# Optimization experiments

Hardware: AMD Instinct MI355X
Metric: run time of the kernel (lower is better)

## Reference

```python
import jax, jax.numpy as jnp
import numpy as np

N, E, H, NH, CUTOFF = 20000, 320000, 128, 8, 5.0
HD = H // NH
EPS = 1e-8
act = jax.nn.silu


def setup_inputs() -> dict:
    key = jax.random.key(0)
    ks = jax.random.split(key, 20)
    g = 1.0 / np.sqrt(H)
    return {
        'node_scalar': jax.random.normal(ks[0], (N, H), jnp.float32),
        'node_vector': jax.random.normal(ks[1], (N, 3, H), jnp.float32),
        'edge_index': jax.random.randint(ks[2], (2, E), 0, N),
        'dist': jax.random.uniform(ks[3], (E,), jnp.float32) * CUTOFF,
        'edge_feats': jax.random.normal(ks[4], (E, H), jnp.float32),
        'edge_vector': jax.random.normal(ks[5], (E, 3), jnp.float32),
        'ln_gamma': jnp.ones((H,), jnp.float32),
        'ln_beta': jnp.zeros((H,), jnp.float32),
        'alpha': jax.random.normal(ks[6], (1, NH, HD), jnp.float32) * g,
        'W_cross': jax.random.normal(ks[7], (H, H), jnp.float32) * g,
        'W_node': jax.random.normal(ks[8], (H, H), jnp.float32) * g,
        'b_node': jnp.zeros((H,), jnp.float32),
        'W_edge': jax.random.normal(ks[9], (H, H), jnp.float32) * g,
        'b_edge': jnp.zeros((H,), jnp.float32),
        'W_p1': jax.random.normal(ks[10], (H, 2 * H), jnp.float32) * g,
        'b_p1': jnp.zeros((2 * H,), jnp.float32),
        'W_p2': jax.random.normal(ks[11], (H, 3 * H), jnp.float32) * g,
        'b_p2': jnp.zeros((3 * H,), jnp.float32),
        'W_vec': jax.random.normal(ks[12], (H, 2 * H), jnp.float32) * g,
        'W_f': jax.random.normal(ks[13], (H, H), jnp.float32) * g,
        'b_f': jnp.zeros((H,), jnp.float32),
    }


def _layernorm(x, gamma, beta):
    mu = jnp.mean(x, axis=-1, keepdims=True)
    var = jnp.var(x, axis=-1, keepdims=True)
    return (x - mu) * jax.lax.rsqrt(var + 1e-5) * gamma + beta


def _cutoff(d):
    return 0.5 * (jnp.cos(jnp.pi * d / CUTOFF) + 1.0) * (d < CUTOFF).astype(d.dtype)


def reference(node_scalar, node_vector, edge_index, dist, edge_feats, edge_vector,
              ln_gamma, ln_beta, alpha, W_cross, W_node, b_node, W_edge, b_edge,
              W_p1, b_p1, W_p2, b_p2, W_vec, W_f, b_f):
    i, j = edge_index[0], edge_index[1]

    scalar_out = _layernorm(node_scalar, ln_gamma, ln_beta)

    # ---- message ----
    ef = act(edge_feats @ W_edge + b_edge).reshape(E, NH, HD)
    ns = (scalar_out @ W_node + b_node).reshape(N, NH, HD)
    attn = act(ns[i] + ns[j] + ef) * alpha            # [E,NH,HD]
    attn = attn.sum(-1) * _cutoff(dist)[:, None]      # [E,NH]
    msg = (ns[j] * ef * attn[:, :, None]).reshape(E, H)
    s1, s2 = jnp.split(act(msg @ W_p1 + b_p1), 2, axis=1)
    vmsg = node_vector[j] * s1[:, None, :] + s2[:, None, :] * edge_vector[:, :, None]
    scalar_agg = jax.ops.segment_sum(msg, i, num_segments=N)
    vector_agg = jax.ops.segment_sum(vmsg, i, num_segments=N)

    # ---- edge update ----
    nv = node_vector @ W_cross                        # [N,3,H]
    ci = jnp.cross(nv[i], edge_vector[:, :, None], axis=1)
    cj = jnp.cross(nv[j], edge_vector[:, :, None], axis=1)
    sum_phi = (ci * cj).sum(1)                        # [E,H]
    edge_feats_out = edge_feats + act(edge_feats @ W_f + b_f) * sum_phi

    node_scalar = node_scalar + scalar_agg
    node_vector = node_vector + vector_agg

    # ---- node update ----
    v1, v2 = jnp.split(node_vector @ W_vec, 2, axis=-1)  # [N,3,H] each
    vec_tri = (v1 * v2).sum(1)                           # [N,H]
    norm_vec = jnp.sqrt((v2 ** 2).sum(-2) + EPS)
    vec_qua = norm_vec ** 3
    p1, p2, p3 = jnp.split(node_scalar @ W_p2 + b_p2, 3, axis=1)
    delta_scalar = (vec_qua + vec_tri) * p1 + p2
    delta_vector = v1 * p3[:, None, :]

    node_scalar = node_scalar + delta_scalar
    node_vector = node_vector + delta_vector
    return node_scalar, node_vector, edge_feats_out
```

## Files before the change

### kernel.cpp

```cpp
#include <hip/hip_runtime.h>

#define N_NODES 20000
#define N_EDGES 320000
#define HDIM    128
#define PI_F    3.14159265358979323846f
#define CUTOFF_R 5.0f

__device__ __forceinline__ float silu_f(float x) {
    return x / (1.0f + __expf(-x));
}

__global__ __launch_bounds__(256) void ln_kernel(
    const float* __restrict__ x, const float* __restrict__ gamma,
    const float* __restrict__ beta, float* __restrict__ out)
{
    int row  = blockIdx.x * 4 + (threadIdx.x >> 6);
    int lane = threadIdx.x & 63;
    if (row >= N_NODES) return;
    const float* xr = x + row * HDIM;
    float x0 = xr[lane], x1 = xr[lane + 64];
    float s  = x0 + x1;
    float s2 = x0 * x0 + x1 * x1;
#pragma unroll
    for (int m = 32; m >= 1; m >>= 1) {
        s  += __shfl_xor(s,  m, 64);
        s2 += __shfl_xor(s2, m, 64);
    }
    float mean = s * (1.0f / 128.0f);
    float var  = s2 * (1.0f / 128.0f) - mean * mean;
    float rstd = rsqrtf(var + 1e-5f);
    out[row * HDIM + lane]      = (x0 - mean) * rstd * gamma[lane]      + beta[lane];
    out[row * HDIM + lane + 64] = (x1 - mean) * rstd * gamma[lane + 64] + beta[lane + 64];
}

template <bool SILU, bool BIAS>
__global__ __launch_bounds__(256) void gemm_k128(
    const float* __restrict__ A, const float* __restrict__ W,
    const float* __restrict__ bias, float* __restrict__ out,
    int M, int C)
{
    __shared__ float As[64][33];
    __shared__ float Ws[32][128];

    int tid = threadIdx.x;
    int tx = tid & 15, ty = tid >> 4;
    int m0 = blockIdx.x * 64;
    int n0 = blockIdx.y * 128;

    float acc[4][8];
#pragma unroll
    for (int r = 0; r < 4; ++r)
#pragma unroll
        for (int c = 0; c < 8; ++c) acc[r][c] = 0.0f;

    for (int k0 = 0; k0 < 128; k0 += 32) {
        __syncthreads();
#pragma unroll
        for (int p = 0; p < 2; ++p) {
            int f  = tid + p * 256;
            int ar = f >> 3, k4 = (f & 7) * 4;
            int gr = m0 + ar;
            float4 v = (gr < M) ? *(const float4*)&A[gr * 128 + k0 + k4]
                                : make_float4(0.f, 0.f, 0.f, 0.f);
            As[ar][k4 + 0] = v.x; As[ar][k4 + 1] = v.y;
            As[ar][k4 + 2] = v.z; As[ar][k4 + 3] = v.w;
        }
#pragma unroll
        for (int p = 0; p < 4; ++p) {
            int f  = tid + p * 256;
            int kr = f >> 5, c4 = (f & 31) * 4;
            *(float4*)&Ws[kr][c4] = *(const float4*)&W[(k0 + kr) * C + n0 + c4];
        }
        __syncthreads();
#pragma unroll 8
        for (int k = 0; k < 32; ++k) {
            float av[4];
#pragma unroll
            for (int r = 0; r < 4; ++r) av[r] = As[ty * 4 + r][k];
            float4 w0 = *(float4*)&Ws[k][tx * 8];
            float4 w1 = *(float4*)&Ws[k][tx * 8 + 4];
            float wv[8] = {w0.x, w0.y, w0.z, w0.w, w1.x, w1.y, w1.z, w1.w};
#pragma unroll
            for (int r = 0; r < 4; ++r)
#pragma unroll
                for (int c = 0; c < 8; ++c) acc[r][c] += av[r] * wv[c];
        }
    }
#pragma unroll
    for (int r = 0; r < 4; ++r) {
        int gr = m0 + ty * 4 + r;
        if (gr < M) {
            float res[8];
#pragma unroll
            for (int c = 0; c < 8; ++c) {
                float v = acc[r][c];
                if (BIAS) v += bias[n0 + tx * 8 + c];
                if (SILU) v = silu_f(v);
                res[c] = v;
            }
            *(float4*)&out[gr * C + n0 + tx * 8]     = make_float4(res[0], res[1], res[2], res[3]);
            *(float4*)&out[gr * C + n0 + tx * 8 + 4] = make_float4(res[4], res[5], res[6], res[7]);
        }
    }
}

__global__ __launch_bounds__(256) void edge_msg_kernel(
    float* __restrict__ efmsg, const float* __restrict__ ns,
    const int* __restrict__ eidx, const float* __restrict__ dist,
    const float* __restrict__ alpha, float* __restrict__ sagg)
{
    int e = blockIdx.x * 2 + (threadIdx.x >> 7);
    int h = threadIdx.x & 127;
    int i = eidx[e], j = eidx[N_EDGES + e];
    float ef  = efmsg[e * HDIM + h];
    float nsi = ns[i * HDIM + h];
    float nsj = ns[j * HDIM + h];
    float pre = silu_f(nsi + nsj + ef) * alpha[h];
#pragma unroll
    for (int m = 8; m >= 1; m >>= 1) pre += __shfl_xor(pre, m, 16);
    float d   = dist[e];
    float cut = (d < CUTOFF_R) ? 0.5f * (cosf(PI_F * d * (1.0f / CUTOFF_R)) + 1.0f) : 0.0f;
    float msg = nsj * ef * (pre * cut);
    efmsg[e * HDIM + h] = msg;
    atomicAdd(&sagg[i * HDIM + h], msg);
}

__global__ __launch_bounds__(256) void gemm_p1_vmsg(
    const float* __restrict__ Amsg, const float* __restrict__ Wp1,
    const float* __restrict__ bp1, const float* __restrict__ node_vector,
    const int* __restrict__ eidx, const float* __restrict__ edge_vector,
    float* __restrict__ vagg)
{
    __shared__ float As[32][33];
    __shared__ float Ws[32][256];
    __shared__ int   ei_s[32], ej_s[32];
    __shared__ float ev_s[32][3];

    int tid = threadIdx.x;
    int tx = tid & 31, ty = tid >> 5;
    int e0 = blockIdx.x * 32;

    if (tid < 32) { ei_s[tid] = eidx[e0 + tid]; ej_s[tid] = eidx[N_EDGES + e0 + tid]; }
    if (tid >= 64 && tid < 160) {
        int t = tid - 64;
        ev_s[t / 3][t % 3] = edge_vector[e0 * 3 + t];
    }

    float acc[4][8];
#pragma unroll
    for (int r = 0; r < 4; ++r)
#pragma unroll
        for (int c = 0; c < 8; ++c) acc[r][c] = 0.0f;

    for (int k0 = 0; k0 < 128; k0 += 32) {
        __syncthreads();
        {
            int ar = tid >> 3, k4 = (tid & 7) * 4;
            float4 v = *(const float4*)&Amsg[(e0 + ar) * 128 + k0 + k4];
            As[ar][k4 + 0] = v.x; As[ar][k4 + 1] = v.y;
            As[ar][k4 + 2] = v.z; As[ar][k4 + 3] = v.w;
        }
#pragma unroll
        for (int p = 0; p < 8; ++p) {
            int f  = tid + p * 256;
            int kr = f >> 6, c4 = (f & 63) * 4;
            *(float4*)&Ws[kr][c4] = *(const float4*)&Wp1[(k0 + kr) * 256 + c4];
        }
        __syncthreads();
#pragma unroll 8
        for (int k = 0; k < 32; ++k) {
            float av[4];
#pragma unroll
            for (int r = 0; r < 4; ++r) av[r] = As[ty * 4 + r][k];
            float4 w0 = *(float4*)&Ws[k][tx * 8];
            float4 w1 = *(float4*)&Ws[k][tx * 8 + 4];
            float wv[8] = {w0.x, w0.y, w0.z, w0.w, w1.x, w1.y, w1.z, w1.w};
#pragma unroll
            for (int r = 0; r < 4; ++r)
#pragma unroll
                for (int c = 0; c < 8; ++c) acc[r][c] += av[r] * wv[c];
        }
    }
    __syncthreads();
#pragma unroll
    for (int r = 0; r < 4; ++r)
#pragma unroll
        for (int c = 0; c < 8; ++c)
            Ws[ty * 4 + r][tx * 8 + c] = silu_f(acc[r][c] + bp1[tx * 8 + c]);
    __syncthreads();

#pragma unroll
    for (int p = 0; p < 16; ++p) {
        int idx = tid + p * 256;
        int r = idx >> 7, h = idx & 127;
        float s1 = Ws[r][h], s2 = Ws[r][h + 128];
        int i = ei_s[r], j = ej_s[r];
#pragma unroll
        for (int d = 0; d < 3; ++d) {
            float v = node_vector[(j * 3 + d) * 128 + h] * s1 + s2 * ev_s[r][d];
            atomicAdd(&vagg[(i * 3 + d) * 128 + h], v);
        }
    }
}

__global__ __launch_bounds__(256) void gemm_wf_edgeout(
    const float* __restrict__ edge_feats, const float* __restrict__ Wf,
    const float* __restrict__ bf, const float* __restrict__ nvg,
    const int* __restrict__ eidx, const float* __restrict__ edge_vector,
    float* __restrict__ edge_out)
{
    __shared__ float As[64][33];
    __shared__ float Ws[32][128];
    __shared__ int   ei_s[64], ej_s[64];
    __shared__ float ev_s[64][3];

    int tid = threadIdx.x;
    int tx = tid & 15, ty = tid >> 4;
    int e0 = blockIdx.x * 64;

    if (tid < 64) { ei_s[tid] = eidx[e0 + tid]; ej_s[tid] = eidx[N_EDGES + e0 + tid]; }
    if (tid >= 64 && tid < 256) {
        int t = tid - 64;
        if (t < 192) ev_s[t / 3][t % 3] = edge_vector[e0 * 3 + t];
    }

    float acc[4][8];
#pragma unroll
    for (int r = 0; r < 4; ++r)
#pragma unroll
        for (int c = 0; c < 8; ++c) acc[r][c] = 0.0f;

    for (int k0 = 0; k0 < 128; k0 += 32) {
        __syncthreads();
#pragma unroll
        for (int p = 0; p < 2; ++p) {
            int f  = tid + p * 256;
            int ar = f >> 3, k4 = (f & 7) * 4;
            float4 v = *(const float4*)&edge_feats[(e0 + ar) * 128 + k0 + k4];
            As[ar][k4 + 0] = v.x; As[ar][k4 + 1] = v.y;
            As[ar][k4 + 2] = v.z; As[ar][k4 + 3] = v.w;
        }
#pragma unroll
        for (int p = 0; p < 4; ++p) {
            int f  = tid + p * 256;
            int kr = f >> 5, c4 = (f & 31) * 4;
            *(float4*)&Ws[kr][c4] = *(const float4*)&Wf[(k0 + kr) * 128 + c4];
        }
        __syncthreads();
#pragma unroll 8
        for (int k = 0; k < 32; ++k) {
            float av[4];
#pragma unroll
            for (int r = 0; r < 4; ++r) av[r] = As[ty * 4 + r][k];
            float4 w0 = *(float4*)&Ws[k][tx * 8];
            float4 w1 = *(float4*)&Ws[k][tx * 8 + 4];
            float wv[8] = {w0.x, w0.y, w0.z, w0.w, w1.x, w1.y, w1.z, w1.w};
#pragma unroll
            for (int r = 0; r < 4; ++r)
#pragma unroll
                for (int c = 0; c < 8; ++c) acc[r][c] += av[r] * wv[c];
        }
    }

#pragma unroll
    for (int r = 0; r < 4; ++r) {
        int row = ty * 4 + r;
        int e   = e0 + row;
        int i = ei_s[row], j = ej_s[row];
        float ev0 = ev_s[row][0], ev1 = ev_s[row][1], ev2 = ev_s[row][2];
        float nvi[3][8], nvj[3][8];
#pragma unroll
        for (int d = 0; d < 3; ++d) {
            float4 a0 = *(const float4*)&nvg[(i * 3 + d) * 128 + tx * 8];
            float4 a1 = *(const float4*)&nvg[(i * 3 + d) * 128 + tx * 8 + 4];
            nvi[d][0] = a0.x; nvi[d][1] = a0.y; nvi[d][2] = a0.z; nvi[d][3] = a0.w;
            nvi[d][4] = a1.x; nvi[d][5] = a1.y; nvi[d][6] = a1.z; nvi[d][7] = a1.w;
            float4 b0 = *(const float4*)&nvg[(j * 3 + d) * 128 + tx * 8];
            float4 b1 = *(const float4*)&nvg[(j * 3 + d) * 128 + tx * 8 + 4];
            nvj[d][0] = b0.x; nvj[d][1] = b0.y; nvj[d][2] = b0.z; nvj[d][3] = b0.w;
            nvj[d][4] = b1.x; nvj[d][5] = b1.y; nvj[d][6] = b1.z; nvj[d][7] = b1.w;
        }
        float4 f0 = *(const float4*)&edge_feats[e * 128 + tx * 8];
        float4 f1 = *(const float4*)&edge_feats[e * 128 + tx * 8 + 4];
        float efres[8] = {f0.x, f0.y, f0.z, f0.w, f1.x, f1.y, f1.z, f1.w};
        float res[8];
#pragma unroll
        for (int c = 0; c < 8; ++c) {
            float ci0 = nvi[1][c] * ev2 - nvi[2][c] * ev1;
            float ci1 = nvi[2][c] * ev0 - nvi[0][c] * ev2;
            float ci2 = nvi[0][c] * ev1 - nvi[1][c] * ev0;
            float cj0 = nvj[1][c] * ev2 - nvj[2][c] * ev1;
            float cj1 = nvj[2][c] * ev0 - nvj[0][c] * ev2;
            float cj2 = nvj[0][c] * ev1 - nvj[1][c] * ev0;
            float sp  = ci0 * cj0 + ci1 * cj1 + ci2 * cj2;
            float t   = silu_f(acc[r][c] + bf[tx * 8 + c]);
            res[c] = efres[c] + t * sp;
        }
        *(float4*)&edge_out[e * 128 + tx * 8]     = make_float4(res[0], res[1], res[2], res[3]);
        *(float4*)&edge_out[e * 128 + tx * 8 + 4] = make_float4(res[4], res[5], res[6], res[7]);
    }
}

__global__ __launch_bounds__(256) void node_add_kernel(
    const float* __restrict__ ns0, const float* __restrict__ sagg,
    const float* __restrict__ nv0, const float* __restrict__ vagg,
    float* __restrict__ ns_new, float* __restrict__ nv_new)
{
    int idx = blockIdx.x * 256 + threadIdx.x;
    const int nsf4 = N_NODES * HDIM / 4;
    if (idx < nsf4) {
        float4 a = ((const float4*)ns0)[idx];
        float4 b = ((const float4*)sagg)[idx];
        ((float4*)ns_new)[idx] = make_float4(a.x + b.x, a.y + b.y, a.z + b.z, a.w + b.w);
    } else {
        int k = idx - nsf4;
        float4 a = ((const float4*)nv0)[k];
        float4 b = ((const float4*)vagg)[k];
        ((float4*)nv_new)[k] = make_float4(a.x + b.x, a.y + b.y, a.z + b.z, a.w + b.w);
    }
}

__global__ __launch_bounds__(256) void final_node_kernel(
    const float* __restrict__ v12, const float* __restrict__ p123,
    const float* __restrict__ ns_new, const float* __restrict__ nv_new,
    float* __restrict__ out_s, float* __restrict__ out_v)
{
    int idx = blockIdx.x * 256 + threadIdx.x;
    int n = idx >> 7, h = idx & 127;
    float tri = 0.f, q2 = 0.f;
    float v1d[3];
#pragma unroll
    for (int d = 0; d < 3; ++d) {
        float v1 = v12[(n * 3 + d) * 256 + h];
        float v2 = v12[(n * 3 + d) * 256 + 128 + h];
        v1d[d] = v1;
        tri += v1 * v2;
        q2  += v2 * v2;
    }
    float nrm = sqrtf(q2 + 1e-8f);
    float qua = nrm * nrm * nrm;
    float p1 = p123[n * 384 + h];
    float p2 = p123[n * 384 + 128 + h];
    float p3 = p123[n * 384 + 256 + h];
    out_s[idx] = ns_new[idx] + (qua + tri) * p1 + p2;
#pragma unroll
    for (int d = 0; d < 3; ++d)
        out_v[(n * 3 + d) * 128 + h] = nv_new[(n * 3 + d) * 128 + h] + v1d[d] * p3;
}

extern "C" void kernel_launch(void* const* d_in, const int* in_sizes, int n_in,
                              void* d_out, int out_size, void* d_ws, size_t ws_size,
                              hipStream_t stream)
{
    const float* node_scalar = (const float*)d_in[0];
    const float* node_vector = (const float*)d_in[1];
    const int*   edge_index  = (const int*)d_in[2];
    const float* dist        = (const float*)d_in[3];
    const float* edge_feats  = (const float*)d_in[4];
    const float* edge_vector = (const float*)d_in[5];
    const float* ln_gamma    = (const float*)d_in[6];
    const float* ln_beta     = (const float*)d_in[7];
    const float* alpha       = (const float*)d_in[8];
    const float* W_cross     = (const float*)d_in[9];
    const float* W_node      = (const float*)d_in[10];
    const float* b_node      = (const float*)d_in[11];
    const float* W_edge      = (const float*)d_in[12];
    const float* b_edge      = (const float*)d_in[13];
    const float* W_p1        = (const float*)d_in[14];
    const float* b_p1        = (const float*)d_in[15];
    const float* W_p2        = (const float*)d_in[16];
    const float* b_p2        = (const float*)d_in[17];
    const float* W_vec       = (const float*)d_in[18];
    const float* W_f         = (const float*)d_in[19];
    const float* b_f         = (const float*)d_in[20];

    float* out_scalar = (float*)d_out;
    float* out_vector = out_scalar + N_NODES * HDIM;
    float* out_edge   = out_vector + N_NODES * 3 * HDIM;

    float* ws         = (float*)d_ws;
    float* scalar_out = ws;
    float* ns         = scalar_out + 2560000;
    float* nv         = ns + 2560000;
    float* sagg       = nv + 7680000;
    float* vagg       = sagg + 2560000;
    float* efmsg      = vagg + 7680000;
    float* v12        = efmsg;
    float* p123       = efmsg + 15360000;

    hipMemsetAsync(sagg, 0, (size_t)(2560000 + 7680000) * sizeof(float), stream);

    hipLaunchKernelGGL(ln_kernel, dim3(5000), dim3(256), 0, stream,
                       node_scalar, ln_gamma, ln_beta, scalar_out);
    hipLaunchKernelGGL((gemm_k128<false, true>), dim3(313, 1), dim3(256), 0, stream,
                       scalar_out, W_node, b_node, ns, N_NODES, 128);
    hipLaunchKernelGGL((gemm_k128<false, false>), dim3(938, 1), dim3(256), 0, stream,
                       node_vector, W_cross, nullptr, nv, 3 * N_NODES, 128);

    hipLaunchKernelGGL((gemm_k128<true, true>), dim3(5000, 1), dim3(256), 0, stream,
                       edge_feats, W_edge, b_edge, efmsg, N_EDGES, 128);
    hipLaunchKernelGGL(edge_msg_kernel, dim3(160000), dim3(256), 0, stream,
                       efmsg, ns, edge_index, dist, alpha, sagg);
    hipLaunchKernelGGL(gemm_p1_vmsg, dim3(10000), dim3(256), 0, stream,
                       efmsg, W_p1, b_p1, node_vector, edge_index, edge_vector, vagg);
    hipLaunchKernelGGL(gemm_wf_edgeout, dim3(5000), dim3(256), 0, stream,
                       edge_feats, W_f, b_f, nv, edge_index, edge_vector, out_edge);

    hipLaunchKernelGGL(node_add_kernel, dim3(10000), dim3(256), 0, stream,
                       node_scalar, sagg, node_vector, vagg, scalar_out, nv);
    hipLaunchKernelGGL((gemm_k128<false, false>), dim3(938, 2), dim3(256), 0, stream,
                       nv, W_vec, nullptr, v12, 3 * N_NODES, 256);
    hipLaunchKernelGGL((gemm_k128<false, true>), dim3(313, 3), dim3(256), 0, stream,
                       scalar_out, W_p2, b_p2, p123, N_NODES, 384);
    hipLaunchKernelGGL(final_node_kernel, dim3(10000), dim3(256), 0, stream,
                       v12, p123, scalar_out, nv, out_scalar, out_vector);
}
```

Before: 1.560 ms.

## Sort edges by destination, fuse edge GEMM with message, pre-reduce atomics, enlarge GEMM tiles

```diff
diff --git a/kernel.cpp b/kernel.cpp
--- a/kernel.cpp
+++ b/kernel.cpp
@@ -6,8 +6,9 @@
 #define PI_F    3.14159265358979323846f
 #define CUTOFF_R 5.0f
 
-__device__ __forceinline__ float silu_f(float x) {
-    return x / (1.0f + __expf(-x));
+__device__ __forceinline__ float silu_f(float x) { return x / (1.0f + __expf(-x)); }
+__device__ __forceinline__ float cutoff_f(float d) {
+    return (d < CUTOFF_R) ? 0.5f * (__cosf(PI_F * d * (1.0f / CUTOFF_R)) + 1.0f) : 0.0f;
 }
 
 __global__ __launch_bounds__(256) void ln_kernel(
@@ -17,7 +18,7 @@
     int row  = blockIdx.x * 4 + (threadIdx.x >> 6);
     int lane = threadIdx.x & 63;
     if (row >= N_NODES) return;
-    const float* xr = x + row * HDIM;
+    const float* xr = x + (size_t)row * HDIM;
     float x0 = xr[lane], x1 = xr[lane + 64];
     float s  = x0 + x1;
     float s2 = x0 * x0 + x1 * x1;
@@ -33,256 +34,399 @@
     out[row * HDIM + lane + 64] = (x1 - mean) * rstd * gamma[lane + 64] + beta[lane + 64];
 }
 
-template <bool SILU, bool BIAS>
-__global__ __launch_bounds__(256) void gemm_k128(
+__global__ __launch_bounds__(256) void count_kernel(const int* __restrict__ ei, int* __restrict__ cnt) {
+    int e = blockIdx.x * 256 + threadIdx.x;
+    if (e < N_EDGES) atomicAdd(&cnt[ei[e]], 1);
+}
+
+__global__ __launch_bounds__(1024) void scan_kernel(const int* __restrict__ cnt, int* __restrict__ ofs) {
+    __shared__ int part[1024];
+    int tid = threadIdx.x;
+    const int PER = 20;
+    int base = tid * PER;
+    int s = 0;
+    for (int t = 0; t < PER; ++t) { int b = base + t; if (b < N_NODES) s += cnt[b]; }
+    part[tid] = s;
+    __syncthreads();
+    for (int off = 1; off < 1024; off <<= 1) {
+        int v = (tid >= off) ? part[tid - off] : 0;
+        __syncthreads();
+        part[tid] += v;
+        __syncthreads();
+    }
+    int run = (tid > 0) ? part[tid - 1] : 0;
+    for (int t = 0; t < PER; ++t) {
+        int b = base + t;
+        if (b < N_NODES) { ofs[b] = run; run += cnt[b]; }
+    }
+}
+
+__global__ __launch_bounds__(256) void scatter_kernel(const int* __restrict__ ei,
+                                                      int* __restrict__ ofs, int* __restrict__ perm) {
+    int e = blockIdx.x * 256 + threadIdx.x;
+    if (e < N_EDGES) { int p = atomicAdd(&ofs[ei[e]], 1); perm[p] = e; }
+}
+
+template <bool BIAS>
+__global__ __launch_bounds__(256) void gemm128_v2(
     const float* __restrict__ A, const float* __restrict__ W,
-    const float* __restrict__ bias, float* __restrict__ out,
-    int M, int C)
-{
-    __shared__ float As[64][33];
+    const float* __restrict__ bias, float* __restrict__ out, int M, int C)
+{
+    __shared__ float At[32][132];
     __shared__ float Ws[32][128];
-
-    int tid = threadIdx.x;
-    int tx = tid & 15, ty = tid >> 4;
-    int m0 = blockIdx.x * 64;
-    int n0 = blockIdx.y * 128;
-
-    float acc[4][8];
-#pragma unroll
-    for (int r = 0; r < 4; ++r)
-#pragma unroll
-        for (int c = 0; c < 8; ++c) acc[r][c] = 0.0f;
+    int tid = threadIdx.x, tx = tid & 15, ty = tid >> 4;
+    int m0 = blockIdx.x * 128, n0 = blockIdx.y * 128;
+    float acc[8][8];
+#pragma unroll
+    for (int r = 0; r < 8; ++r)
+#pragma unroll
+        for (int c = 0; c < 8; ++c) acc[r][c] = 0.f;
 
     for (int k0 = 0; k0 < 128; k0 += 32) {
         __syncthreads();
 #pragma unroll
-        for (int p = 0; p < 2; ++p) {
-            int f  = tid + p * 256;
-            int ar = f >> 3, k4 = (f & 7) * 4;
-            int gr = m0 + ar;
-            float4 v = (gr < M) ? *(const float4*)&A[gr * 128 + k0 + k4]
+        for (int p = 0; p < 4; ++p) {
+            int f = tid + p * 256, ar = f >> 3, k4 = (f & 7) * 4, gr = m0 + ar;
+            float4 v = (gr < M) ? *(const float4*)&A[(size_t)gr * 128 + k0 + k4]
                                 : make_float4(0.f, 0.f, 0.f, 0.f);
-            As[ar][k4 + 0] = v.x; As[ar][k4 + 1] = v.y;
-            As[ar][k4 + 2] = v.z; As[ar][k4 + 3] = v.w;
+            At[k4 + 0][ar] = v.x; At[k4 + 1][ar] = v.y;
+            At[k4 + 2][ar] = v.z; At[k4 + 3][ar] = v.w;
         }
 #pragma unroll
         for (int p = 0; p < 4; ++p) {
-            int f  = tid + p * 256;
-            int kr = f >> 5, c4 = (f & 31) * 4;
-            *(float4*)&Ws[kr][c4] = *(const float4*)&W[(k0 + kr) * C + n0 + c4];
-        }
-        __syncthreads();
-#pragma unroll 8
+            int f = tid + p * 256, kr = f >> 5, c4 = (f & 31) * 4;
+            *(float4*)&Ws[kr][c4] = *(const float4*)&W[(size_t)(k0 + kr) * C + n0 + c4];
+        }
+        __syncthreads();
+#pragma unroll
         for (int k = 0; k < 32; ++k) {
-            float av[4];
-#pragma unroll
-            for (int r = 0; r < 4; ++r) av[r] = As[ty * 4 + r][k];
-            float4 w0 = *(float4*)&Ws[k][tx * 8];
-            float4 w1 = *(float4*)&Ws[k][tx * 8 + 4];
+            float4 a0 = *(const float4*)&At[k][ty * 8], a1 = *(const float4*)&At[k][ty * 8 + 4];
+            float4 w0 = *(const float4*)&Ws[k][tx * 8], w1 = *(const float4*)&Ws[k][tx * 8 + 4];
+            float av[8] = {a0.x, a0.y, a0.z, a0.w, a1.x, a1.y, a1.z, a1.w};
             float wv[8] = {w0.x, w0.y, w0.z, w0.w, w1.x, w1.y, w1.z, w1.w};
 #pragma unroll
-            for (int r = 0; r < 4; ++r)
+            for (int r = 0; r < 8; ++r)
 #pragma unroll
                 for (int c = 0; c < 8; ++c) acc[r][c] += av[r] * wv[c];
         }
     }
-#pragma unroll
-    for (int r = 0; r < 4; ++r) {
-        int gr = m0 + ty * 4 + r;
+    float bv[8];
+    if (BIAS) {
+        float4 b0 = *(const float4*)&bias[n0 + tx * 8], b1 = *(const float4*)&bias[n0 + tx * 8 + 4];
+        bv[0] = b0.x; bv[1] = b0.y; bv[2] = b0.z; bv[3] = b0.w;
+        bv[4] = b1.x; bv[5] = b1.y; bv[6] = b1.z; bv[7] = b1.w;
+    }
+#pragma unroll
+    for (int r = 0; r < 8; ++r) {
+        int gr = m0 + ty * 8 + r;
         if (gr < M) {
             float res[8];
 #pragma unroll
-            for (int c = 0; c < 8; ++c) {
-                float v = acc[r][c];
-                if (BIAS) v += bias[n0 + tx * 8 + c];
-                if (SILU) v = silu_f(v);
-                res[c] = v;
-            }
-            *(float4*)&out[gr * C + n0 + tx * 8]     = make_float4(res[0], res[1], res[2], res[3]);
-            *(float4*)&out[gr * C + n0 + tx * 8 + 4] = make_float4(res[4], res[5], res[6], res[7]);
-        }
-    }
-}
-
-__global__ __launch_bounds__(256) void edge_msg_kernel(
-    float* __restrict__ efmsg, const float* __restrict__ ns,
+            for (int c = 0; c < 8; ++c) { float v = acc[r][c]; if (BIAS) v += bv[c]; res[c] = v; }
+            *(float4*)&out[(size_t)gr * C + n0 + tx * 8]     = make_float4(res[0], res[1], res[2], res[3]);
+            *(float4*)&out[(size_t)gr * C + n0 + tx * 8 + 4] = make_float4(res[4], res[5], res[6], res[7]);
+        }
+    }
+}
+
+__global__ __launch_bounds__(256) void k1_edge_gemm_msg(
+    const float* __restrict__ edge_feats, const float* __restrict__ We,
+    const float* __restrict__ be, const float* __restrict__ ns,
     const int* __restrict__ eidx, const float* __restrict__ dist,
-    const float* __restrict__ alpha, float* __restrict__ sagg)
-{
-    int e = blockIdx.x * 2 + (threadIdx.x >> 7);
-    int h = threadIdx.x & 127;
-    int i = eidx[e], j = eidx[N_EDGES + e];
-    float ef  = efmsg[e * HDIM + h];
-    float nsi = ns[i * HDIM + h];
-    float nsj = ns[j * HDIM + h];
-    float pre = silu_f(nsi + nsj + ef) * alpha[h];
-#pragma unroll
-    for (int m = 8; m >= 1; m >>= 1) pre += __shfl_xor(pre, m, 16);
-    float d   = dist[e];
-    float cut = (d < CUTOFF_R) ? 0.5f * (cosf(PI_F * d * (1.0f / CUTOFF_R)) + 1.0f) : 0.0f;
-    float msg = nsj * ef * (pre * cut);
-    efmsg[e * HDIM + h] = msg;
-    atomicAdd(&sagg[i * HDIM + h], msg);
-}
-
-__global__ __launch_bounds__(256) void gemm_p1_vmsg(
-    const float* __restrict__ Amsg, const float* __restrict__ Wp1,
+    const float* __restrict__ alpha, const int* __restrict__ perm,
+    float* __restrict__ msg, float* __restrict__ sagg)
+{
+    __shared__ float At[32][132];
+    __shared__ float Ws[32][128];
+    __shared__ int perm_s[128], i_s[128], j_s[128];
+    __shared__ float d_s[128];
+    int tid = threadIdx.x, tx = tid & 15, ty = tid >> 4;
+    int e0 = blockIdx.x * 128;
+
+    if (tid < 128) perm_s[tid] = perm[e0 + tid];
+    __syncthreads();
+    if (tid < 128) {
+        int pe = perm_s[tid];
+        i_s[tid] = eidx[pe]; j_s[tid] = eidx[N_EDGES + pe]; d_s[tid] = dist[pe];
+    }
+
+    float acc[8][8];
+#pragma unroll
+    for (int r = 0; r < 8; ++r)
+#pragma unroll
+        for (int c = 0; c < 8; ++c) acc[r][c] = 0.f;
+
+    for (int k0 = 0; k0 < 128; k0 += 32) {
+        __syncthreads();
+#pragma unroll
+        for (int p = 0; p < 4; ++p) {
+            int f = tid + p * 256, ar = f >> 3, k4 = (f & 7) * 4;
+            int gr = perm_s[ar];
+            float4 v = *(const float4*)&edge_feats[(size_t)gr * 128 + k0 + k4];
+            At[k4 + 0][ar] = v.x; At[k4 + 1][ar] = v.y;
+            At[k4 + 2][ar] = v.z; At[k4 + 3][ar] = v.w;
+        }
+#pragma unroll
+        for (int p = 0; p < 4; ++p) {
+            int f = tid + p * 256, kr = f >> 5, c4 = (f & 31) * 4;
+            *(float4*)&Ws[kr][c4] = *(const float4*)&We[(size_t)(k0 + kr) * 128 + c4];
+        }
+        __syncthreads();
+#pragma unroll
+        for (int k = 0; k < 32; ++k) {
+            float4 a0 = *(const float4*)&At[k][ty * 8], a1 = *(const float4*)&At[k][ty * 8 + 4];
+            float4 w0 = *(const float4*)&Ws[k][tx * 8], w1 = *(const float4*)&Ws[k][tx * 8 + 4];
+            float av[8] = {a0.x, a0.y, a0.z, a0.w, a1.x, a1.y, a1.z, a1.w};
+            float wv[8] = {w0.x, w0.y, w0.z, w0.w, w1.x, w1.y, w1.z, w1.w};
+#pragma unroll
+            for (int r = 0; r < 8; ++r)
+#pragma unroll
+                for (int c = 0; c < 8; ++c) acc[r][c] += av[r] * wv[c];
+        }
+    }
+
+    float bev[8], al[8];
+    {
+        float4 b0 = *(const float4*)&be[tx * 8], b1 = *(const float4*)&be[tx * 8 + 4];
+        bev[0]=b0.x; bev[1]=b0.y; bev[2]=b0.z; bev[3]=b0.w; bev[4]=b1.x; bev[5]=b1.y; bev[6]=b1.z; bev[7]=b1.w;
+        float4 a0 = *(const float4*)&alpha[tx * 8], a1 = *(const float4*)&alpha[tx * 8 + 4];
+        al[0]=a0.x; al[1]=a0.y; al[2]=a0.z; al[3]=a0.w; al[4]=a1.x; al[5]=a1.y; al[6]=a1.z; al[7]=a1.w;
+    }
+    int cur = i_s[ty * 8];
+    float sac[8];
+#pragma unroll
+    for (int c = 0; c < 8; ++c) sac[c] = 0.f;
+
+    auto flush = [&](void) {
+#pragma unroll
+        for (int c = 0; c < 8; ++c) atomicAdd(&sagg[(size_t)cur * 128 + tx * 8 + c], sac[c]);
+#pragma unroll
+        for (int c = 0; c < 8; ++c) sac[c] = 0.f;
+    };
+
+#pragma unroll
+    for (int r = 0; r < 8; ++r) {
+        int row = ty * 8 + r;
+        int gi = i_s[row], gj = j_s[row];
+        float efv[8];
+#pragma unroll
+        for (int c = 0; c < 8; ++c) efv[c] = silu_f(acc[r][c] + bev[c]);
+        const float* nip = &ns[(size_t)gi * 128 + tx * 8];
+        const float* njp = &ns[(size_t)gj * 128 + tx * 8];
+        float4 ni0 = *(const float4*)nip, ni1 = *(const float4*)(nip + 4);
+        float4 nj0 = *(const float4*)njp, nj1 = *(const float4*)(njp + 4);
+        float niv[8] = {ni0.x, ni0.y, ni0.z, ni0.w, ni1.x, ni1.y, ni1.z, ni1.w};
+        float njv[8] = {nj0.x, nj0.y, nj0.z, nj0.w, nj1.x, nj1.y, nj1.z, nj1.w};
+        float ps = 0.f;
+#pragma unroll
+        for (int c = 0; c < 8; ++c) ps += silu_f(niv[c] + njv[c] + efv[c]) * al[c];
+        float hs = ps + __shfl_xor(ps, 1, 64);
+        float attn = hs * cutoff_f(d_s[row]);
+        float mv[8];
+#pragma unroll
+        for (int c = 0; c < 8; ++c) mv[c] = njv[c] * efv[c] * attn;
+        *(float4*)&msg[(size_t)(e0 + row) * 128 + tx * 8]     = make_float4(mv[0], mv[1], mv[2], mv[3]);
+        *(float4*)&msg[(size_t)(e0 + row) * 128 + tx * 8 + 4] = make_float4(mv[4], mv[5], mv[6], mv[7]);
+        if (gi != cur) { flush(); cur = gi; }
+#pragma unroll
+        for (int c = 0; c < 8; ++c) sac[c] += mv[c];
+    }
+    flush();
+}
+
+__global__ __launch_bounds__(256) void k2_p1_vmsg(
+    const float* __restrict__ msg, const float* __restrict__ Wp1,
     const float* __restrict__ bp1, const float* __restrict__ node_vector,
     const int* __restrict__ eidx, const float* __restrict__ edge_vector,
-    float* __restrict__ vagg)
-{
-    __shared__ float As[32][33];
+    const int* __restrict__ perm, float* __restrict__ vagg)
+{
+    __shared__ float At[32][68];
     __shared__ float Ws[32][256];
-    __shared__ int   ei_s[32], ej_s[32];
-    __shared__ float ev_s[32][3];
-
-    int tid = threadIdx.x;
-    int tx = tid & 31, ty = tid >> 5;
-    int e0 = blockIdx.x * 32;
-
-    if (tid < 32) { ei_s[tid] = eidx[e0 + tid]; ej_s[tid] = eidx[N_EDGES + e0 + tid]; }
-    if (tid >= 64 && tid < 160) {
+    __shared__ int perm_s[64], i_s[64], j_s[64];
+    __shared__ float ev_s[64][3];
+    int tid = threadIdx.x, tx = tid & 31, ty = tid >> 5;
+    int e0 = blockIdx.x * 64;
+
+    if (tid < 64) perm_s[tid] = perm[e0 + tid];
+    __syncthreads();
+    if (tid < 64) {
+        int pe = perm_s[tid];
+        i_s[tid] = eidx[pe]; j_s[tid] = eidx[N_EDGES + pe];
+    } else {
         int t = tid - 64;
-        ev_s[t / 3][t % 3] = edge_vector[e0 * 3 + t];
-    }
-
-    float acc[4][8];
-#pragma unroll
-    for (int r = 0; r < 4; ++r)
-#pragma unroll
-        for (int c = 0; c < 8; ++c) acc[r][c] = 0.0f;
+        if (t < 192) { int el = t / 3, cm = t - el * 3; ev_s[el][cm] = edge_vector[(size_t)perm_s[el] * 3 + cm]; }
+    }
+
+    float acc[8][8];
+#pragma unroll
+    for (int r = 0; r < 8; ++r)
+#pragma unroll
+        for (int c = 0; c < 8; ++c) acc[r][c] = 0.f;
 
     for (int k0 = 0; k0 < 128; k0 += 32) {
         __syncthreads();
-        {
-            int ar = tid >> 3, k4 = (tid & 7) * 4;
-            float4 v = *(const float4*)&Amsg[(e0 + ar) * 128 + k0 + k4];
-            As[ar][k4 + 0] = v.x; As[ar][k4 + 1] = v.y;
-            As[ar][k4 + 2] = v.z; As[ar][k4 + 3] = v.w;
+#pragma unroll
+        for (int p = 0; p < 2; ++p) {
+            int f = tid + p * 256, ar = f >> 3, k4 = (f & 7) * 4;
+            float4 v = *(const float4*)&msg[(size_t)(e0 + ar) * 128 + k0 + k4];
+            At[k4 + 0][ar] = v.x; At[k4 + 1][ar] = v.y;
+            At[k4 + 2][ar] = v.z; At[k4 + 3][ar] = v.w;
         }
 #pragma unroll
         for (int p = 0; p < 8; ++p) {
-            int f  = tid + p * 256;
-            int kr = f >> 6, c4 = (f & 63) * 4;
-            *(float4*)&Ws[kr][c4] = *(const float4*)&Wp1[(k0 + kr) * 256 + c4];
-        }
-        __syncthreads();
-#pragma unroll 8
+            int f = tid + p * 256, kr = f >> 6, c4 = (f & 63) * 4;
+            *(float4*)&Ws[kr][c4] = *(const float4*)&Wp1[(size_t)(k0 + kr) * 256 + c4];
+        }
+        __syncthreads();
+#pragma unroll
         for (int k = 0; k < 32; ++k) {
-            float av[4];
-#pragma unroll
-            for (int r = 0; r < 4; ++r) av[r] = As[ty * 4 + r][k];
-            float4 w0 = *(float4*)&Ws[k][tx * 8];
-            float4 w1 = *(float4*)&Ws[k][tx * 8 + 4];
+            float4 a0 = *(const float4*)&At[k][ty * 8], a1 = *(const float4*)&At[k][ty * 8 + 4];
+            float4 w0 = *(const float4*)&Ws[k][tx * 8], w1 = *(const float4*)&Ws[k][tx * 8 + 4];
+            float av[8] = {a0.x, a0.y, a0.z, a0.w, a1.x, a1.y, a1.z, a1.w};
             float wv[8] = {w0.x, w0.y, w0.z, w0.w, w1.x, w1.y, w1.z, w1.w};
 #pragma unroll
-            for (int r = 0; r < 4; ++r)
+            for (int r = 0; r < 8; ++r)
 #pragma unroll
                 for (int c = 0; c < 8; ++c) acc[r][c] += av[r] * wv[c];
         }
     }
-    __syncthreads();
-#pragma unroll
-    for (int r = 0; r < 4; ++r)
-#pragma unroll
-        for (int c = 0; c < 8; ++c)
-            Ws[ty * 4 + r][tx * 8 + c] = silu_f(acc[r][c] + bp1[tx * 8 + c]);
-    __syncthreads();
-
-#pragma unroll
-    for (int p = 0; p < 16; ++p) {
-        int idx = tid + p * 256;
-        int r = idx >> 7, h = idx & 127;
-        float s1 = Ws[r][h], s2 = Ws[r][h + 128];
-        int i = ei_s[r], j = ej_s[r];
-#pragma unroll
-        for (int d = 0; d < 3; ++d) {
-            float v = node_vector[(j * 3 + d) * 128 + h] * s1 + s2 * ev_s[r][d];
-            atomicAdd(&vagg[(i * 3 + d) * 128 + h], v);
-        }
-    }
-}
-
-__global__ __launch_bounds__(256) void gemm_wf_edgeout(
+
+    float bv[8];
+    {
+        float4 b0 = *(const float4*)&bp1[tx * 8], b1 = *(const float4*)&bp1[tx * 8 + 4];
+        bv[0]=b0.x; bv[1]=b0.y; bv[2]=b0.z; bv[3]=b0.w; bv[4]=b1.x; bv[5]=b1.y; bv[6]=b1.z; bv[7]=b1.w;
+    }
+    bool lo = (tx < 16);
+    int h0 = (tx & 15) * 8;
+    int cur = i_s[ty * 8];
+    float va0[8], va1[8];
+#pragma unroll
+    for (int c = 0; c < 8; ++c) { va0[c] = 0.f; va1[c] = 0.f; }
+
+    auto flushv = [&](void) {
+        if (lo) {
+#pragma unroll
+            for (int c = 0; c < 8; ++c) atomicAdd(&vagg[((size_t)cur * 3 + 0) * 128 + h0 + c], va0[c]);
+#pragma unroll
+            for (int c = 0; c < 8; ++c) atomicAdd(&vagg[((size_t)cur * 3 + 1) * 128 + h0 + c], va1[c]);
+        } else {
+#pragma unroll
+            for (int c = 0; c < 8; ++c) atomicAdd(&vagg[((size_t)cur * 3 + 2) * 128 + h0 + c], va0[c]);
+        }
+#pragma unroll
+        for (int c = 0; c < 8; ++c) { va0[c] = 0.f; va1[c] = 0.f; }
+    };
+
+#pragma unroll
+    for (int r = 0; r < 8; ++r) {
+        int row = ty * 8 + r;
+        int gi = i_s[row], gj = j_s[row];
+        float sv[8], ov[8];
+#pragma unroll
+        for (int c = 0; c < 8; ++c) sv[c] = silu_f(acc[r][c] + bv[c]);
+#pragma unroll
+        for (int c = 0; c < 8; ++c) ov[c] = __shfl_xor(sv[c], 16, 64);
+        float s1[8], s2[8];
+#pragma unroll
+        for (int c = 0; c < 8; ++c) { s1[c] = lo ? sv[c] : ov[c]; s2[c] = lo ? ov[c] : sv[c]; }
+        if (gi != cur) { flushv(); cur = gi; }
+        const float* nvb = &node_vector[(size_t)gj * 3 * 128 + h0];
+        if (lo) {
+            float ev0 = ev_s[row][0], ev1 = ev_s[row][1];
+            float4 a0 = *(const float4*)&nvb[0],       a1 = *(const float4*)&nvb[4];
+            float4 b0 = *(const float4*)&nvb[128],     b1 = *(const float4*)&nvb[132];
+            float na[8] = {a0.x, a0.y, a0.z, a0.w, a1.x, a1.y, a1.z, a1.w};
+            float nb[8] = {b0.x, b0.y, b0.z, b0.w, b1.x, b1.y, b1.z, b1.w};
+#pragma unroll
+            for (int c = 0; c < 8; ++c) { va0[c] += na[c] * s1[c] + s2[c] * ev0; va1[c] += nb[c] * s1[c] + s2[c] * ev1; }
+        } else {
+            float ev2 = ev_s[row][2];
+            float4 a0 = *(const float4*)&nvb[256],     a1 = *(const float4*)&nvb[260];
+            float na[8] = {a0.x, a0.y, a0.z, a0.w, a1.x, a1.y, a1.z, a1.w};
+#pragma unroll
+            for (int c = 0; c < 8; ++c) va0[c] += na[c] * s1[c] + s2[c] * ev2;
+        }
+    }
+    flushv();
+}
+
+__global__ __launch_bounds__(256) void k3_wf_edgeout(
     const float* __restrict__ edge_feats, const float* __restrict__ Wf,
     const float* __restrict__ bf, const float* __restrict__ nvg,
     const int* __restrict__ eidx, const float* __restrict__ edge_vector,
     float* __restrict__ edge_out)
 {
-    __shared__ float As[64][33];
+    __shared__ float At[32][132];
     __shared__ float Ws[32][128];
-    __shared__ int   ei_s[64], ej_s[64];
-    __shared__ float ev_s[64][3];
-
-    int tid = threadIdx.x;
-    int tx = tid & 15, ty = tid >> 4;
-    int e0 = blockIdx.x * 64;
-
-    if (tid < 64) { ei_s[tid] = eidx[e0 + tid]; ej_s[tid] = eidx[N_EDGES + e0 + tid]; }
-    if (tid >= 64 && tid < 256) {
-        int t = tid - 64;
-        if (t < 192) ev_s[t / 3][t % 3] = edge_vector[e0 * 3 + t];
-    }
-
-    float acc[4][8];
-#pragma unroll
-    for (int r = 0; r < 4; ++r)
-#pragma unroll
-        for (int c = 0; c < 8; ++c) acc[r][c] = 0.0f;
+    __shared__ int i_s[128], j_s[128];
+    __shared__ float evf[384];
+    int tid = threadIdx.x, tx = tid & 15, ty = tid >> 4;
+    int e0 = blockIdx.x * 128;
+
+    if (tid < 128) { i_s[tid] = eidx[e0 + tid]; j_s[tid] = eidx[N_EDGES + e0 + tid]; }
+    evf[tid < 256 ? tid : 0] = edge_vector[(size_t)e0 * 3 + (tid < 256 ? tid : 0)];
+    if (tid < 128) evf[256 + tid] = edge_vector[(size_t)e0 * 3 + 256 + tid];
+
+    float acc[8][8];
+#pragma unroll
+    for (int r = 0; r < 8; ++r)
+#pragma unroll
+        for (int c = 0; c < 8; ++c) acc[r][c] = 0.f;
 
     for (int k0 = 0; k0 < 128; k0 += 32) {
         __syncthreads();
 #pragma unroll
-        for (int p = 0; p < 2; ++p) {
-            int f  = tid + p * 256;
-            int ar = f >> 3, k4 = (f & 7) * 4;
-            float4 v = *(const float4*)&edge_feats[(e0 + ar) * 128 + k0 + k4];
-            As[ar][k4 + 0] = v.x; As[ar][k4 + 1] = v.y;
-            As[ar][k4 + 2] = v.z; As[ar][k4 + 3] = v.w;
-        }
-#pragma unroll
         for (int p = 0; p < 4; ++p) {
-            int f  = tid + p * 256;
-            int kr = f >> 5, c4 = (f & 31) * 4;
-            *(float4*)&Ws[kr][c4] = *(const float4*)&Wf[(k0 + kr) * 128 + c4];
-        }
-        __syncthreads();
-#pragma unroll 8
+            int f = tid + p * 256, ar = f >> 3, k4 = (f & 7) * 4;
+            float4 v = *(const float4*)&edge_feats[(size_t)(e0 + ar) * 128 + k0 + k4];
+            At[k4 + 0][ar] = v.x; At[k4 + 1][ar] = v.y;
+            At[k4 + 2][ar] = v.z; At[k4 + 3][ar] = v.w;
+        }
+#pragma unroll
+        for (int p = 0; p < 4; ++p) {
+            int f = tid + p * 256, kr = f >> 5, c4 = (f & 31) * 4;
+            *(float4*)&Ws[kr][c4] = *(const float4*)&Wf[(size_t)(k0 + kr) * 128 + c4];
+        }
+        __syncthreads();
+#pragma unroll
         for (int k = 0; k < 32; ++k) {
-            float av[4];
-#pragma unroll
-            for (int r = 0; r < 4; ++r) av[r] = As[ty * 4 + r][k];
-            float4 w0 = *(float4*)&Ws[k][tx * 8];
-            float4 w1 = *(float4*)&Ws[k][tx * 8 + 4];
+            float4 a0 = *(const float4*)&At[k][ty * 8], a1 = *(const float4*)&At[k][ty * 8 + 4];
+            float4 w0 = *(const float4*)&Ws[k][tx * 8], w1 = *(const float4*)&Ws[k][tx * 8 + 4];
+            float av[8] = {a0.x, a0.y, a0.z, a0.w, a1.x, a1.y, a1.z, a1.w};
             float wv[8] = {w0.x, w0.y, w0.z, w0.w, w1.x, w1.y, w1.z, w1.w};
 #pragma unroll
-            for (int r = 0; r < 4; ++r)
+            for (int r = 0; r < 8; ++r)
 #pragma unroll
                 for (int c = 0; c < 8; ++c) acc[r][c] += av[r] * wv[c];
         }
     }
 
-#pragma unroll
-    for (int r = 0; r < 4; ++r) {
-        int row = ty * 4 + r;
-        int e   = e0 + row;
-        int i = ei_s[row], j = ej_s[row];
-        float ev0 = ev_s[row][0], ev1 = ev_s[row][1], ev2 = ev_s[row][2];
+    float bfv[8];
+    {
+        float4 b0 = *(const float4*)&bf[tx * 8], b1 = *(const float4*)&bf[tx * 8 + 4];
+        bfv[0]=b0.x; bfv[1]=b0.y; bfv[2]=b0.z; bfv[3]=b0.w; bfv[4]=b1.x; bfv[5]=b1.y; bfv[6]=b1.z; bfv[7]=b1.w;
+    }
+#pragma unroll
+    for (int r = 0; r < 8; ++r) {
+        int row = ty * 8 + r;
+        int e = e0 + row;
+        int gi = i_s[row], gj = j_s[row];
+        float ev0 = evf[row * 3 + 0], ev1 = evf[row * 3 + 1], ev2 = evf[row * 3 + 2];
         float nvi[3][8], nvj[3][8];
 #pragma unroll
         for (int d = 0; d < 3; ++d) {
-            float4 a0 = *(const float4*)&nvg[(i * 3 + d) * 128 + tx * 8];
-            float4 a1 = *(const float4*)&nvg[(i * 3 + d) * 128 + tx * 8 + 4];
-            nvi[d][0] = a0.x; nvi[d][1] = a0.y; nvi[d][2] = a0.z; nvi[d][3] = a0.w;
-            nvi[d][4] = a1.x; nvi[d][5] = a1.y; nvi[d][6] = a1.z; nvi[d][7] = a1.w;
-            float4 b0 = *(const float4*)&nvg[(j * 3 + d) * 128 + tx * 8];
-            float4 b1 = *(const float4*)&nvg[(j * 3 + d) * 128 + tx * 8 + 4];
-            nvj[d][0] = b0.x; nvj[d][1] = b0.y; nvj[d][2] = b0.z; nvj[d][3] = b0.w;
-            nvj[d][4] = b1.x; nvj[d][5] = b1.y; nvj[d][6] = b1.z; nvj[d][7] = b1.w;
-        }
-        float4 f0 = *(const float4*)&edge_feats[e * 128 + tx * 8];
-        float4 f1 = *(const float4*)&edge_feats[e * 128 + tx * 8 + 4];
-        float efres[8] = {f0.x, f0.y, f0.z, f0.w, f1.x, f1.y, f1.z, f1.w};
+            const float* pi = &nvg[((size_t)gi * 3 + d) * 128 + tx * 8];
+            const float* pj = &nvg[((size_t)gj * 3 + d) * 128 + tx * 8];
+            float4 a0 = *(const float4*)pi, a1 = *(const float4*)(pi + 4);
+            float4 b0 = *(const float4*)pj, b1 = *(const float4*)(pj + 4);
+            nvi[d][0]=a0.x; nvi[d][1]=a0.y; nvi[d][2]=a0.z; nvi[d][3]=a0.w;
+            nvi[d][4]=a1.x; nvi[d][5]=a1.y; nvi[d][6]=a1.z; nvi[d][7]=a1.w;
+            nvj[d][0]=b0.x; nvj[d][1]=b0.y; nvj[d][2]=b0.z; nvj[d][3]=b0.w;
+            nvj[d][4]=b1.x; nvj[d][5]=b1.y; nvj[d][6]=b1.z; nvj[d][7]=b1.w;
+        }
+        float4 f0 = *(const float4*)&edge_feats[(size_t)e * 128 + tx * 8];
+        float4 f1 = *(const float4*)&edge_feats[(size_t)e * 128 + tx * 8 + 4];
+        float efr[8] = {f0.x, f0.y, f0.z, f0.w, f1.x, f1.y, f1.z, f1.w};
         float res[8];
 #pragma unroll
         for (int c = 0; c < 8; ++c) {
@@ -293,11 +437,10 @@
             float cj1 = nvj[2][c] * ev0 - nvj[0][c] * ev2;
             float cj2 = nvj[0][c] * ev1 - nvj[1][c] * ev0;
             float sp  = ci0 * cj0 + ci1 * cj1 + ci2 * cj2;
-            float t   = silu_f(acc[r][c] + bf[tx * 8 + c]);
-            res[c] = efres[c] + t * sp;
-        }
-        *(float4*)&edge_out[e * 128 + tx * 8]     = make_float4(res[0], res[1], res[2], res[3]);
-        *(float4*)&edge_out[e * 128 + tx * 8 + 4] = make_float4(res[4], res[5], res[6], res[7]);
+            res[c] = efr[c] + silu_f(acc[r][c] + bfv[c]) * sp;
+        }
+        *(float4*)&edge_out[(size_t)e * 128 + tx * 8]     = make_float4(res[0], res[1], res[2], res[3]);
+        *(float4*)&edge_out[(size_t)e * 128 + tx * 8 + 4] = make_float4(res[4], res[5], res[6], res[7]);
     }
 }
 
@@ -331,21 +474,21 @@
     float v1d[3];
 #pragma unroll
     for (int d = 0; d < 3; ++d) {
-        float v1 = v12[(n * 3 + d) * 256 + h];
-        float v2 = v12[(n * 3 + d) * 256 + 128 + h];
+        float v1 = v12[((size_t)n * 3 + d) * 256 + h];
+        float v2 = v12[((size_t)n * 3 + d) * 256 + 128 + h];
         v1d[d] = v1;
         tri += v1 * v2;
         q2  += v2 * v2;
     }
     float nrm = sqrtf(q2 + 1e-8f);
     float qua = nrm * nrm * nrm;
-    float p1 = p123[n * 384 + h];
-    float p2 = p123[n * 384 + 128 + h];
-    float p3 = p123[n * 384 + 256 + h];
+    float p1 = p123[(size_t)n * 384 + h];
+    float p2 = p123[(size_t)n * 384 + 128 + h];
+    float p3 = p123[(size_t)n * 384 + 256 + h];
     out_s[idx] = ns_new[idx] + (qua + tri) * p1 + p2;
 #pragma unroll
     for (int d = 0; d < 3; ++d)
-        out_v[(n * 3 + d) * 128 + h] = nv_new[(n * 3 + d) * 128 + h] + v1d[d] * p3;
+        out_v[((size_t)n * 3 + d) * 128 + h] = nv_new[((size_t)n * 3 + d) * 128 + h] + v1d[d] * p3;
 }
 
 extern "C" void kernel_launch(void* const* d_in, const int* in_sizes, int n_in,
@@ -377,41 +520,47 @@
     float* out_scalar = (float*)d_out;
     float* out_vector = out_scalar + N_NODES * HDIM;
     float* out_edge   = out_vector + N_NODES * 3 * HDIM;
-
-    float* ws         = (float*)d_ws;
-    float* scalar_out = ws;
-    float* ns         = scalar_out + 2560000;
-    float* nv         = ns + 2560000;
-    float* sagg       = nv + 7680000;
-    float* vagg       = sagg + 2560000;
-    float* efmsg      = vagg + 7680000;
-    float* v12        = efmsg;
-    float* p123       = efmsg + 15360000;
+    float* msg        = out_edge;
+
+    float* ws   = (float*)d_ws;
+    float* sc   = ws;
+    float* ns   = ws + 2560000;
+    float* nv   = ws + 5120000;
+    float* sagg = ws + 12800000;
+    float* vagg = ws + 15360000;
+    float* v12  = ws + 23040000;
+    float* p123 = ws + 38400000;
+    int*   perm = (int*)(ws + 46080000);
+    int*   cnt  = (int*)(ws + 46400000);
+    int*   ofs  = (int*)(ws + 46420000);
 
     hipMemsetAsync(sagg, 0, (size_t)(2560000 + 7680000) * sizeof(float), stream);
+    hipMemsetAsync(cnt, 0, (size_t)N_NODES * sizeof(int), stream);
+
+    hipLaunchKernelGGL(count_kernel,   dim3(1250), dim3(256),  0, stream, edge_index, cnt);
+    hipLaunchKernelGGL(scan_kernel,    dim3(1),    dim3(1024), 0, stream, cnt, ofs);
+    hipLaunchKernelGGL(scatter_kernel, dim3(1250), dim3(256),  0, stream, edge_index, ofs, perm);
 
     hipLaunchKernelGGL(ln_kernel, dim3(5000), dim3(256), 0, stream,
-                       node_scalar, ln_gamma, ln_beta, scalar_out);
-    hipLaunchKernelGGL((gemm_k128<false, true>), dim3(313, 1), dim3(256), 0, stream,
-                       scalar_out, W_node, b_node, ns, N_NODES, 128);
-    hipLaunchKernelGGL((gemm_k128<false, false>), dim3(938, 1), dim3(256), 0, stream,
+                       node_scalar, ln_gamma, ln_beta, sc);
+    hipLaunchKernelGGL((gemm128_v2<true>),  dim3(157, 1), dim3(256), 0, stream,
+                       sc, W_node, b_node, ns, N_NODES, 128);
+    hipLaunchKernelGGL((gemm128_v2<false>), dim3(469, 1), dim3(256), 0, stream,
                        node_vector, W_cross, nullptr, nv, 3 * N_NODES, 128);
 
-    hipLaunchKernelGGL((gemm_k128<true, true>), dim3(5000, 1), dim3(256), 0, stream,
-                       edge_feats, W_edge, b_edge, efmsg, N_EDGES, 128);
-    hipLaunchKernelGGL(edge_msg_kernel, dim3(160000), dim3(256), 0, stream,
-                       efmsg, ns, edge_index, dist, alpha, sagg);
-    hipLaunchKernelGGL(gemm_p1_vmsg, dim3(10000), dim3(256), 0, stream,
-                       efmsg, W_p1, b_p1, node_vector, edge_index, edge_vector, vagg);
-    hipLaunchKernelGGL(gemm_wf_edgeout, dim3(5000), dim3(256), 0, stream,
+    hipLaunchKernelGGL(k1_edge_gemm_msg, dim3(2500), dim3(256), 0, stream,
+                       edge_feats, W_edge, b_edge, ns, edge_index, dist, alpha, perm, msg, sagg);
+    hipLaunchKernelGGL(k2_p1_vmsg, dim3(5000), dim3(256), 0, stream,
+                       msg, W_p1, b_p1, node_vector, edge_index, edge_vector, perm, vagg);
+    hipLaunchKernelGGL(k3_wf_edgeout, dim3(2500), dim3(256), 0, stream,
                        edge_feats, W_f, b_f, nv, edge_index, edge_vector, out_edge);
 
     hipLaunchKernelGGL(node_add_kernel, dim3(10000), dim3(256), 0, stream,
-                       node_scalar, sagg, node_vector, vagg, scalar_out, nv);
-    hipLaunchKernelGGL((gemm_k128<false, false>), dim3(938, 2), dim3(256), 0, stream,
+                       node_scalar, sagg, node_vector, vagg, sc, nv);
+    hipLaunchKernelGGL((gemm128_v2<false>), dim3(469, 2), dim3(256), 0, stream,
                        nv, W_vec, nullptr, v12, 3 * N_NODES, 256);
-    hipLaunchKernelGGL((gemm_k128<false, true>), dim3(313, 3), dim3(256), 0, stream,
-                       scalar_out, W_p2, b_p2, p123, N_NODES, 384);
+    hipLaunchKernelGGL((gemm128_v2<true>),  dim3(157, 3), dim3(256), 0, stream,
+                       sc, W_p2, b_p2, p123, N_NODES, 384);
     hipLaunchKernelGGL(final_node_kernel, dim3(10000), dim3(256), 0, stream,
-                       v12, p123, scalar_out, nv, out_scalar, out_vector);
-}
+                       v12, p123, sc, nv, out_scalar, out_vector);
+}
```

New measurement: 1.878 ms. +20.4%, slower.
